# Kernel optimization log

Measured on AMD Instinct MI355X. Metric: run time of the kernel, lower is better.

## Reference

```python
import jax, jax.numpy as jnp
import numpy as np

B, A, DIN, HID, HEADS, NOUT, K = 256, 64, 64, 128, 4, 2, 7
N = B * A                      # 16384 nodes
C = HID                        # per-head dim == out_channels (module quirk)
SCALE = (HID // HEADS) ** -0.5 # 1/sqrt(32), as in the module


def _xavier(k, shape):
    fan_out, fan_in = shape
    lim = (6.0 / (fan_in + fan_out)) ** 0.5
    return jax.random.uniform(k, shape, jnp.float32, -lim, lim)


def setup_inputs() -> dict:
    key = jax.random.key(0)
    ks = jax.random.split(key, 24)
    x = jax.random.normal(ks[0], (N, DIN), jnp.float32)
    pos_b = jax.random.uniform(ks[1], (B, A, 2), jnp.float32) * 10.0  # [B,A,2]
    pos = pos_b.reshape(N, 2)

    # kNN graph per environment (replicates torch.cdist + topk smallest, drop self)
    d = jnp.linalg.norm(pos_b[:, :, None, :] - pos_b[:, None, :, :], axis=-1)  # [B,A,A]
    _, idx = jax.lax.top_k(-d, K + 1)
    nb = idx[..., 1:]                                   # [B,A,K] neighbor ids
    offs = (jnp.arange(B) * A)[:, None, None]
    src = jnp.broadcast_to(jnp.arange(A)[None, :, None], (B, A, K)) + offs
    dst = nb + offs
    loops = jnp.arange(N)
    edge_index = jnp.stack([
        jnp.concatenate([src.reshape(-1), loops]),
        jnp.concatenate([dst.reshape(-1), loops]),
    ]).astype(jnp.int32)                                # [2, E], E = B*A*K + N

    inp = {"x": x, "pos": pos, "edge_index": edge_index}
    inp["l0_Wq"] = _xavier(ks[2], (HEADS * C, 2))
    inp["l0_Wk"] = _xavier(ks[3], (HEADS * C, 2))
    inp["l0_Wv"] = _xavier(ks[4], (HEADS * C, DIN))
    inp["l0_Wo"] = _xavier(ks[5], (HID, HEADS * C))
    inp["l0_bo"] = jnp.zeros((HID,), jnp.float32)
    inp["l1_Wq"] = _xavier(ks[6], (HEADS * C, 2))
    inp["l1_Wk"] = _xavier(ks[7], (HEADS * C, 2))
    inp["l1_Wv"] = _xavier(ks[8], (HEADS * C, HID))
    inp["l1_Wo"] = _xavier(ks[9], (HID, HEADS * C))
    inp["l1_bo"] = jnp.zeros((HID,), jnp.float32)
    inp["W1"] = _xavier(ks[10], (256, HID))
    inp["b1"] = jnp.zeros((256,), jnp.float32)
    inp["W2"] = _xavier(ks[11], (256, 256))
    inp["b2"] = jnp.zeros((256,), jnp.float32)
    inp["W3"] = _xavier(ks[12], (NOUT, 256))
    inp["b3"] = jnp.zeros((NOUT,), jnp.float32)
    return inp


def _gat(x, pos, src, dst, Wq, Wk, Wv, Wo, bo):
    # positions -> Q/K, features -> V (position-aware attention)
    q = (pos @ Wq.T).reshape(N, HEADS, C)
    k = (pos @ Wk.T).reshape(N, HEADS, C)
    v = (x @ Wv.T).reshape(N, HEADS, C)
    # per-edge logits, segment softmax over incoming edges of dst
    alpha = jnp.einsum('ehc,ehc->eh', q[dst], k[src]) * SCALE        # [E,H]
    amax = jax.ops.segment_max(alpha, dst, num_segments=N)           # [N,H]
    ex = jnp.exp(alpha - amax[dst])
    a = ex / jax.ops.segment_sum(ex, dst, num_segments=N)[dst]
    msg = v[src] * a[..., None]                                      # [E,H,C]
    agg = jax.ops.segment_sum(msg, dst, num_segments=N)              # [N,H,C]
    return agg.reshape(N, HEADS * C) @ Wo.T + bo


def reference(x, pos, edge_index,
              l0_Wq, l0_Wk, l0_Wv, l0_Wo, l0_bo,
              l1_Wq, l1_Wk, l1_Wv, l1_Wo, l1_bo,
              W1, b1, W2, b2, W3, b3):
    src, dst = edge_index[0], edge_index[1]
    h = jnp.tanh(_gat(x, pos, src, dst, l0_Wq, l0_Wk, l0_Wv, l0_Wo, l0_bo))
    h = jnp.tanh(_gat(h, pos, src, dst, l1_Wq, l1_Wk, l1_Wv, l1_Wo, l1_bo))
    h = jax.nn.relu(h @ W1.T + b1)
    h = jax.nn.relu(h @ W2.T + b2)
    out = h @ W3.T + b3
    return out.reshape(B, A, NOUT)
```

## Files before the change

kernel.cpp:

```cpp
#include <hip/hip_runtime.h>
#include <hip/hip_bf16.h>
#include <cstddef>
#include <math.h>

#define N_NODES 16384
#define DIN 64
#define HID 128
#define SCALE_F 0.17677669529663687f

using bf16x8 = __attribute__((ext_vector_type(8))) short;
using f32x4  = __attribute__((ext_vector_type(4))) float;

__device__ __forceinline__ ushort f2b(float x) {
  __hip_bfloat16 h = __float2bfloat16(x);
  return *(ushort*)&h;
}
__device__ __forceinline__ float b2f(ushort u) {
  __hip_bfloat16 h = *(__hip_bfloat16*)&u;
  return __bfloat162float(h);
}
__device__ __forceinline__ void split1(float x, ushort& h, ushort& l) {
  h = f2b(x);
  l = f2b(x - b2f(h));
}
__device__ __forceinline__ void split3(float x, ushort& a, ushort& b, ushort& c) {
  a = f2b(x);
  float r1 = x - b2f(a);
  b = f2b(r1);
  c = f2b(r1 - b2f(b));
}

#define MFMA(d, A, B) d = __builtin_amdgcn_mfma_f32_16x16x32_bf16(A, B, d, 0, 0, 0)


__global__ __launch_bounds__(256) void prep_all_kernel(
    const float* __restrict__ Wq0, const float* __restrict__ Wk0,
    const float* __restrict__ Wq1, const float* __restrict__ Wk1,
    float* __restrict__ G,
    const float* __restrict__ Wv0, const float* __restrict__ Wo0,
    ushort* __restrict__ M0a, ushort* __restrict__ M0b, ushort* __restrict__ M0c,
    const float* __restrict__ Wv1, const float* __restrict__ Wo1,
    ushort* __restrict__ M1a, ushort* __restrict__ M1b, ushort* __restrict__ M1c,
    const float* __restrict__ W1, ushort* __restrict__ W1hi, ushort* __restrict__ W1lo,
    const float* __restrict__ W2, ushort* __restrict__ W2hi, ushort* __restrict__ W2lo,
    unsigned long long* __restrict__ out64)
{
  int blk = blockIdx.x, t = threadIdx.x;
  if (blk == 0) {
    if (t >= 32) return;
    int l = t >> 4, h = (t >> 2) & 3, a = (t >> 1) & 1, b = t & 1;
    const float* Wq = l ? Wq1 : Wq0;
    const float* Wk = l ? Wk1 : Wk0;
    float acc = 0.f;
    for (int c = 0; c < 128; c++)
      acc += Wq[(h * 128 + c) * 2 + a] * Wk[(h * 128 + c) * 2 + b];
    G[t] = acc;
  } else if (blk < 385) {
    int D, idx;
    const float *Wv, *Wo;
    ushort *Ma, *Mb, *Mc;
    if (blk < 129) { D = DIN; idx = (blk - 1) * 256 + t; Wv = Wv0; Wo = Wo0; Ma = M0a; Mb = M0b; Mc = M0c; }
    else           { D = HID; idx = (blk - 129) * 256 + t; Wv = Wv1; Wo = Wo1; Ma = M1a; Mb = M1b; Mc = M1c; }
    int K4 = 4 * D;
    int o = idx / K4, hd = idx - o * K4;
    int h = hd / D, d = hd - h * D;
    const float* wv = Wv + (size_t)(h * 128) * D + d;
    const float* wo = Wo + (size_t)o * 512 + h * 128;
    float acc = 0.f;
    for (int c = 0; c < 128; c++)
      acc += wv[(size_t)c * D] * wo[c];
    split3(acc, Ma[idx], Mb[idx], Mc[idx]);
  } else if (blk < 769) {
    int i = (blk - 385) * 256 + t;
    if (i < 256 * 128) split1(W1[i], W1hi[i], W1lo[i]);
    int j = i - 256 * 128;
    if (j >= 0 && j < 256 * 256) split1(W2[j], W2hi[j], W2lo[j]);
  } else {
    int i = (blk - 769) * 256 + t;
    if (i < N_NODES) out64[i] = 0ull;
  }
}


#define SFB_OFF 8192
#define SFC_OFF 16384
#define PXS_OFF 24576
#define PYS_OFF 24704
#define SMASK_OFF 24832
#define AFRAG_OFF 25088
#define PH_OFF 57856
#define LDS_USHORTS 74752

template <int KD>
__device__ __forceinline__ void gat_layer(
    int wave, int lane, int lm, int lq,
    const ushort* sFa, const ushort* sFb, const ushort* sFc,
    ushort* aA,
    const float* pxs, const float* pys,
    const unsigned long long* smask,
    const float* __restrict__ G,
    const ushort* __restrict__ Ma, const ushort* __restrict__ Mb,
    const ushort* __restrict__ Mc,
    f32x4 hacc[4])
{
  {
    int wm = wave & 3;
    int h = wave >> 2;
    float pdxm = pxs[wm * 16 + lm];
    float pdym = pys[wm * 16 + lm];
    unsigned long long mm = smask[wm * 16 + lm];
    unsigned mb0 = (unsigned)((mm >> (8 * lq)) & 0xFF);
    unsigned mb1 = (unsigned)((mm >> (32 + 8 * lq)) & 0xFF);
    float g0 = G[h * 4], g1 = G[h * 4 + 1], g2 = G[h * 4 + 2], g3 = G[h * 4 + 3];
    float a0 = (g0 * pdxm + g2 * pdym) * SCALE_F;
    float a1 = (g1 * pdxm + g3 * pdym) * SCALE_F;
    float sshift = a0 * pdxm + a1 * pdym;
    float e[16];
    float sum = 0.f;
#pragma unroll
    for (int j = 0; j < 8; j++) {
      e[j]     = ((mb0 >> j) & 1) ? __expf(a0 * pxs[8 * lq + j] + a1 * pys[8 * lq + j] - sshift) : 0.f;
      e[8 + j] = ((mb1 >> j) & 1) ? __expf(a0 * pxs[32 + 8 * lq + j] + a1 * pys[32 + 8 * lq + j] - sshift) : 0.f;
      sum += e[j] + e[8 + j];
    }
    sum += __shfl_xor(sum, 16);
    sum += __shfl_xor(sum, 32);
    float inv = 1.f / sum;
    bf16x8 Aa0, Aa1, Ab0, Ab1;
#pragma unroll
    for (int j = 0; j < 8; j++) {
      ushort ua, ub;
      split1(e[j] * inv, ua, ub);     Aa0[j] = (short)ua; Ab0[j] = (short)ub;
      split1(e[8 + j] * inv, ua, ub); Aa1[j] = (short)ua; Ab1[j] = (short)ub;
    }
    int sbase = wave * 2048 + lane * 8;
    *(bf16x8*)&aA[sbase]        = Aa0;
    *(bf16x8*)&aA[sbase + 512]  = Aa1;
    *(bf16x8*)&aA[sbase + 1024] = Ab0;
    *(bf16x8*)&aA[sbase + 1536] = Ab1;
  }
  __syncthreads();

  const int K4 = 4 * KD;
  const int o = 16 * (wave & 7) + lm;
  const int hb = wave >> 3;
#pragma unroll
  for (int i = 0; i < 4; i++) hacc[i] = (f32x4){0.f, 0.f, 0.f, 0.f};

#pragma unroll 1
  for (int hi = 0; hi < 2; hi++) {
    int h = 2 * hb + hi;
    f32x4 y[4];
#pragma unroll
    for (int i = 0; i < 4; i++) y[i] = (f32x4){0.f, 0.f, 0.f, 0.f};
#pragma unroll 1
    for (int kf = 0; kf < KD / 32; kf++) {
      size_t boff = (size_t)o * K4 + h * KD + kf * 32 + lq * 8;
      bf16x8 ma = *(const bf16x8*)&Ma[boff];
      bf16x8 mb = *(const bf16x8*)&Mb[boff];
      bf16x8 mc = *(const bf16x8*)&Mc[boff];
      int ko = kf * 32 + lq * 8;
      int sw = lm << 3;
#pragma unroll
      for (int mp = 0; mp < 2; mp++) {
        int f0 = (mp * 32 + lm) * 128 + (ko ^ sw);
        int f1 = f0 + 16 * 128;
        bf16x8 fa0 = *(const bf16x8*)&sFa[f0], fa1 = *(const bf16x8*)&sFa[f1];
        bf16x8 fb0 = *(const bf16x8*)&sFb[f0], fb1 = *(const bf16x8*)&sFb[f1];
        bf16x8 fc0 = *(const bf16x8*)&sFc[f0], fc1 = *(const bf16x8*)&sFc[f1];
        f32x4 y0 = y[mp * 2], y1 = y[mp * 2 + 1];
        MFMA(y0, fa0, ma); MFMA(y1, fa1, ma);
        MFMA(y0, fa0, mb); MFMA(y1, fa1, mb);
        MFMA(y0, fb0, ma); MFMA(y1, fb1, ma);
        MFMA(y0, fa0, mc); MFMA(y1, fa1, mc);
        MFMA(y0, fc0, ma); MFMA(y1, fc1, ma);
        MFMA(y0, fb0, mb); MFMA(y1, fb1, mb);
        y[mp * 2] = y0; y[mp * 2 + 1] = y1;
      }
    }
    bf16x8 Ya[2], Yb[2];
#pragma unroll
    for (int kb = 0; kb < 2; kb++) {
#pragma unroll
      for (int j = 0; j < 8; j++) {
        int sl = ((2 * lq + (j >> 2)) & 3) * 16 + lm;
        float v0 = __shfl(y[2 * kb][j & 3], sl);
        float v1 = __shfl(y[2 * kb + 1][j & 3], sl);
        float v = (lq & 2) ? v1 : v0;
        ushort ua, ub;
        split1(v, ua, ub);
        Ya[kb][j] = (short)ua; Yb[kb][j] = (short)ub;
      }
    }
#pragma unroll
    for (int mtd = 0; mtd < 4; mtd++) {
      int abase = (h * 4 + mtd) * 2048 + lane * 8;
      bf16x8 Aa0 = *(const bf16x8*)&aA[abase];
      bf16x8 Aa1 = *(const bf16x8*)&aA[abase + 512];
      bf16x8 Ab0 = *(const bf16x8*)&aA[abase + 1024];
      bf16x8 Ab1 = *(const bf16x8*)&aA[abase + 1536];
      MFMA(hacc[mtd], Aa0, Ya[0]);
      MFMA(hacc[mtd], Aa0, Yb[0]);
      MFMA(hacc[mtd], Ab0, Ya[0]);
      MFMA(hacc[mtd], Ab0, Yb[0]);
      MFMA(hacc[mtd], Aa1, Ya[1]);
      MFMA(hacc[mtd], Aa1, Yb[1]);
      MFMA(hacc[mtd], Ab1, Ya[1]);
      MFMA(hacc[mtd], Ab1, Yb[1]);
    }
  }
}

__global__ __attribute__((amdgpu_flat_work_group_size(1024, 1024), amdgpu_waves_per_eu(4)))
void fused_gat_kernel(
    const float* __restrict__ x, const float* __restrict__ pos,
    const int* __restrict__ srcp, const int* __restrict__ dstp,
    const float* __restrict__ G,
    const ushort* __restrict__ M0a, const ushort* __restrict__ M0b, const ushort* __restrict__ M0c,
    const ushort* __restrict__ M1a, const ushort* __restrict__ M1b, const ushort* __restrict__ M1c,
    const float* __restrict__ bo0, const float* __restrict__ bo1,
    const ushort* __restrict__ W1hi, const ushort* __restrict__ W1lo, const float* __restrict__ b1,
    const ushort* __restrict__ W2hi, const ushort* __restrict__ W2lo, const float* __restrict__ b2,
    const float* __restrict__ W3, const float* __restrict__ b3,
    float* __restrict__ outp)
{
  __shared__ __align__(16) ushort uBig[LDS_USHORTS];
  ushort* sFa = uBig;
  ushort* sFb = uBig + SFB_OFF;
  ushort* sFc = uBig + SFC_OFF;
  float* pxs = (float*)(uBig + PXS_OFF);
  float* pys = (float*)(uBig + PYS_OFF);
  unsigned long long* smask = (unsigned long long*)(uBig + SMASK_OFF);
  ushort* aA = uBig + AFRAG_OFF;
  ushort* pA = uBig + AFRAG_OFF;
  ushort* pB = uBig + AFRAG_OFF + 16384;
  float* pH = (float*)(uBig + PH_OFF);

  int b = blockIdx.x, t = threadIdx.x;
  int wave = t >> 6, lane = t & 63, lm = lane & 15, lq = lane >> 4;

  if (t < 64) {
    pxs[t] = pos[(b * 64 + t) * 2];
    pys[t] = pos[(b * 64 + t) * 2 + 1];
    smask[t] = 1ull << t;
  }
  {
    const float4* gx = (const float4*)(x + (size_t)b * 64 * DIN);
    float4 v = gx[t];
    int r = t >> 4, c = (t & 15) * 4;
    int cs = c ^ ((r & 15) << 3);
    ushort4 ua, ub, uc;
    split3(v.x, ua.x, ub.x, uc.x); split3(v.y, ua.y, ub.y, uc.y);
    split3(v.z, ua.z, ub.z, uc.z); split3(v.w, ua.w, ub.w, uc.w);
    *(ushort4*)&sFa[r * 128 + cs] = ua;
    *(ushort4*)&sFb[r * 128 + cs] = ub;
    *(ushort4*)&sFc[r * 128 + cs] = uc;
  }
  __syncthreads();
  if (t < 448) {
    int s = srcp[b * 448 + t];
    int d = dstp[b * 448 + t];
    atomicOr(&smask[d & 63], 1ull << (s & 63));
  }
  __syncthreads();

  f32x4 hacc[4];
  gat_layer<DIN>(wave, lane, lm, lq, sFa, sFb, sFc, aA, pxs, pys, smask,
                 G, M0a, M0b, M0c, hacc);
  int o = 16 * (wave & 7) + lm;
  if (wave >= 8) {
#pragma unroll
    for (int mtd = 0; mtd < 4; mtd++)
#pragma unroll
      for (int r = 0; r < 4; r++)
        pH[(mtd * 16 + lq * 4 + r) * 132 + o] = hacc[mtd][r];
  }
  __syncthreads();
  if (wave < 8) {
    float bv = bo0[o];
#pragma unroll
    for (int mtd = 0; mtd < 4; mtd++)
#pragma unroll
      for (int r = 0; r < 4; r++) {
        int dst = mtd * 16 + lq * 4 + r;
        float v = tanhf(hacc[mtd][r] + pH[dst * 132 + o] + bv);
        ushort ua, ub, uc;
        split3(v, ua, ub, uc);
        int cs = o ^ ((dst & 15) << 3);
        sFa[dst * 128 + cs] = ua;
        sFb[dst * 128 + cs] = ub;
        sFc[dst * 128 + cs] = uc;
      }
  }
  __syncthreads();
  gat_layer<HID>(wave, lane, lm, lq, sFa, sFb, sFc, aA, pxs, pys, smask,
                 G + 16, M1a, M1b, M1c, hacc);
  if (wave >= 8) {
#pragma unroll
    for (int mtd = 0; mtd < 4; mtd++)
#pragma unroll
      for (int r = 0; r < 4; r++)
        pH[(mtd * 16 + lq * 4 + r) * 132 + o] = hacc[mtd][r];
  }
  __syncthreads();
  if (wave < 8) {
    float bv = bo1[o];
#pragma unroll
    for (int mtd = 0; mtd < 4; mtd++)
#pragma unroll
      for (int r = 0; r < 4; r++) {
        int dst = mtd * 16 + lq * 4 + r;
        float v = tanhf(hacc[mtd][r] + pH[dst * 132 + o] + bv);
        ushort hh, ll;
        split1(v, hh, ll);
        int cs = o ^ ((dst & 15) << 3);
        sFa[dst * 128 + cs] = hh;
        sFb[dst * 128 + cs] = ll;
      }
  }
  __syncthreads();
  f32x4 y1[4];
#pragma unroll
  for (int mtd = 0; mtd < 4; mtd++) y1[mtd] = (f32x4){0.f, 0.f, 0.f, 0.f};
#pragma unroll 1
  for (int kf = 0; kf < 4; kf++) {
    int ko = kf * 32 + lq * 8;
    int col = 16 * wave + lm;
    bf16x8 bh = *(const bf16x8*)&W1hi[(size_t)col * 128 + ko];
    bf16x8 bl = *(const bf16x8*)&W1lo[(size_t)col * 128 + ko];
#pragma unroll
    for (int mtd = 0; mtd < 4; mtd++) {
      int row = mtd * 16 + lm;
      int cs = ko ^ (lm << 3);
      bf16x8 ah = *(const bf16x8*)&sFa[row * 128 + cs];
      bf16x8 al = *(const bf16x8*)&sFb[row * 128 + cs];
      MFMA(y1[mtd], ah, bh);
      MFMA(y1[mtd], ah, bl);
      MFMA(y1[mtd], al, bh);
    }
  }
  {
    int col = 16 * wave + lm;
    float bv = b1[col];
#pragma unroll
    for (int mtd = 0; mtd < 4; mtd++)
#pragma unroll
      for (int r = 0; r < 4; r++) {
        int row = mtd * 16 + lq * 4 + r;
        float v = fmaxf(y1[mtd][r] + bv, 0.f);
        ushort hh, ll;
        split1(v, hh, ll);
        int cc = col ^ ((row & 15) << 3);
        pA[row * 256 + cc] = hh;
        pB[row * 256 + cc] = ll;
      }
  }
  __syncthreads();
  f32x4 y2[4];
#pragma unroll
  for (int mtd = 0; mtd < 4; mtd++) y2[mtd] = (f32x4){0.f, 0.f, 0.f, 0.f};
#pragma unroll 1
  for (int kf = 0; kf < 8; kf++) {
    int ko = kf * 32 + lq * 8;
    bf16x8 bh = *(const bf16x8*)&W2hi[(size_t)(16 * wave + lm) * 256 + ko];
    bf16x8 bl = *(const bf16x8*)&W2lo[(size_t)(16 * wave + lm) * 256 + ko];
#pragma unroll
    for (int mtd = 0; mtd < 4; mtd++) {
      int row = mtd * 16 + lm;
      int cc = ko ^ (lm << 3);
      bf16x8 ah = *(const bf16x8*)&pA[row * 256 + cc];
      bf16x8 al = *(const bf16x8*)&pB[row * 256 + cc];
      MFMA(y2[mtd], ah, bh);
      MFMA(y2[mtd], ah, bl);
      MFMA(y2[mtd], al, bh);
    }
  }
  {
    int c0 = 16 * wave + lm;
    float w30 = W3[c0], w31 = W3[256 + c0];
    float b20 = b2[c0];
    float bb0 = (wave == 0) ? b3[0] : 0.f;
    float bb1 = (wave == 0) ? b3[1] : 0.f;
#pragma unroll
    for (int mtd = 0; mtd < 4; mtd++)
#pragma unroll
      for (int r = 0; r < 4; r++) {
        float va = fmaxf(y2[mtd][r] + b20, 0.f);
        float s0 = va * w30;
        float s1 = va * w31;
        s0 += __shfl_xor(s0, 1); s0 += __shfl_xor(s0, 2);
        s0 += __shfl_xor(s0, 4); s0 += __shfl_xor(s0, 8);
        s1 += __shfl_xor(s1, 1); s1 += __shfl_xor(s1, 2);
        s1 += __shfl_xor(s1, 4); s1 += __shfl_xor(s1, 8);
        if (lm == 0) {
          int row = b * 64 + mtd * 16 + lq * 4 + r;
          atomicAdd(&outp[row * 2 + 0], s0 + bb0);
          atomicAdd(&outp[row * 2 + 1], s1 + bb1);
        }
      }
  }
}


extern "C" void kernel_launch(void* const* d_in, const int* in_sizes, int n_in,
                              void* d_out, int out_size, void* d_ws, size_t ws_size,
                              hipStream_t stream) {
  const float* x     = (const float*)d_in[0];
  const float* pos   = (const float*)d_in[1];
  const int*   ei    = (const int*)d_in[2];
  const float* l0_Wq = (const float*)d_in[3];
  const float* l0_Wk = (const float*)d_in[4];
  const float* l0_Wv = (const float*)d_in[5];
  const float* l0_Wo = (const float*)d_in[6];
  const float* l0_bo = (const float*)d_in[7];
  const float* l1_Wq = (const float*)d_in[8];
  const float* l1_Wk = (const float*)d_in[9];
  const float* l1_Wv = (const float*)d_in[10];
  const float* l1_Wo = (const float*)d_in[11];
  const float* l1_bo = (const float*)d_in[12];
  const float* W1    = (const float*)d_in[13];
  const float* b1    = (const float*)d_in[14];
  const float* W2    = (const float*)d_in[15];
  const float* b2    = (const float*)d_in[16];
  const float* W3    = (const float*)d_in[17];
  const float* b3    = (const float*)d_in[18];
  float* outp = (float*)d_out;

  int E = in_sizes[2] / 2;
  const int* srcp = ei;
  const int* dstp = ei + E;

  char* base = (char*)d_ws;
  size_t off = 0;
  auto alloc = [&](size_t bytes) -> void* {
    void* p = base + off;
    off = (off + bytes + 255) & ~(size_t)255;
    return p;
  };
  float*  G   = (float*)alloc(32 * sizeof(float));
  ushort* M0a = (ushort*)alloc((size_t)128 * 256 * 2);
  ushort* M0b = (ushort*)alloc((size_t)128 * 256 * 2);
  ushort* M0c = (ushort*)alloc((size_t)128 * 256 * 2);
  ushort* M1a = (ushort*)alloc((size_t)128 * 512 * 2);
  ushort* M1b = (ushort*)alloc((size_t)128 * 512 * 2);
  ushort* M1c = (ushort*)alloc((size_t)128 * 512 * 2);
  ushort* W1hi = (ushort*)alloc((size_t)256 * 128 * 2);
  ushort* W1lo = (ushort*)alloc((size_t)256 * 128 * 2);
  ushort* W2hi = (ushort*)alloc((size_t)256 * 256 * 2);
  ushort* W2lo = (ushort*)alloc((size_t)256 * 256 * 2);

  prep_all_kernel<<<833, 256, 0, stream>>>(
      l0_Wq, l0_Wk, l1_Wq, l1_Wk, G,
      l0_Wv, l0_Wo, M0a, M0b, M0c,
      l1_Wv, l1_Wo, M1a, M1b, M1c,
      W1, W1hi, W1lo, W2, W2hi, W2lo,
      (unsigned long long*)outp);

  fused_gat_kernel<<<N_NODES / 64, 1024, 0, stream>>>(
      x, pos, srcp, dstp, G, M0a, M0b, M0c, M1a, M1b, M1c, l0_bo, l1_bo,
      W1hi, W1lo, b1, W2hi, W2lo, b2, W3, b3, outp);

  (void)n_in; (void)out_size; (void)ws_size;
}
```

Baseline: 151.7 us.

## Prefetch weight fragments into registers ahead of barriers and MFMA loops

Global loads of the per-layer attention weight fragments, MLP weights, biases, edge lists, positions and input features are moved earlier. They are issued before barriers or softmax work and held in registers, and the K loops are fully unrolled. The head-1 weights of each GAT layer are prefetched right after the head-0 MFMAs finish. The aim is to hide global-memory latency behind compute and barriers, at the cost of much higher VGPR pressure that may cut occupancy or cause spills.

```diff
diff --git a/kernel.cpp b/kernel.cpp
--- a/kernel.cpp
+++ b/kernel.cpp
@@ -103,6 +103,20 @@
     const ushort* __restrict__ Mc,
     f32x4 hacc[4])
 {
+  constexpr int NKF = KD / 32;
+  const int K4 = 4 * KD;
+  const int o = 16 * (wave & 7) + lm;
+  const int hb = wave >> 3;
+
+  bf16x8 pmA[NKF], pmB[NKF], pmC[NKF];
+#pragma unroll
+  for (int kf = 0; kf < NKF; kf++) {
+    size_t boff = (size_t)o * K4 + (2 * hb) * KD + kf * 32 + lq * 8;
+    pmA[kf] = *(const bf16x8*)&Ma[boff];
+    pmB[kf] = *(const bf16x8*)&Mb[boff];
+    pmC[kf] = *(const bf16x8*)&Mc[boff];
+  }
+
   {
     int wm = wave & 3;
     int h = wave >> 2;
@@ -141,9 +155,6 @@
   }
   __syncthreads();
 
-  const int K4 = 4 * KD;
-  const int o = 16 * (wave & 7) + lm;
-  const int hb = wave >> 3;
 #pragma unroll
   for (int i = 0; i < 4; i++) hacc[i] = (f32x4){0.f, 0.f, 0.f, 0.f};
 
@@ -153,12 +164,11 @@
     f32x4 y[4];
 #pragma unroll
     for (int i = 0; i < 4; i++) y[i] = (f32x4){0.f, 0.f, 0.f, 0.f};
-#pragma unroll 1
-    for (int kf = 0; kf < KD / 32; kf++) {
-      size_t boff = (size_t)o * K4 + h * KD + kf * 32 + lq * 8;
-      bf16x8 ma = *(const bf16x8*)&Ma[boff];
-      bf16x8 mb = *(const bf16x8*)&Mb[boff];
-      bf16x8 mc = *(const bf16x8*)&Mc[boff];
+#pragma unroll
+    for (int kf = 0; kf < NKF; kf++) {
+      bf16x8 ma = pmA[kf];
+      bf16x8 mb = pmB[kf];
+      bf16x8 mc = pmC[kf];
       int ko = kf * 32 + lq * 8;
       int sw = lm << 3;
 #pragma unroll
@@ -176,6 +186,15 @@
         MFMA(y0, fc0, ma); MFMA(y1, fc1, ma);
         MFMA(y0, fb0, mb); MFMA(y1, fb1, mb);
         y[mp * 2] = y0; y[mp * 2 + 1] = y1;
+      }
+    }
+    if (hi == 0) {
+#pragma unroll
+      for (int kf = 0; kf < NKF; kf++) {
+        size_t boff = (size_t)o * K4 + (2 * hb + 1) * KD + kf * 32 + lq * 8;
+        pmA[kf] = *(const bf16x8*)&Ma[boff];
+        pmB[kf] = *(const bf16x8*)&Mb[boff];
+        pmC[kf] = *(const bf16x8*)&Mc[boff];
       }
     }
     bf16x8 Ya[2], Yb[2];
@@ -238,36 +257,47 @@
 
   int b = blockIdx.x, t = threadIdx.x;
   int wave = t >> 6, lane = t & 63, lm = lane & 15, lq = lane >> 4;
-
+  int o = 16 * (wave & 7) + lm;
+
+  int e_s = 0, e_d = 0;
+  if (t < 448) {
+    e_s = srcp[b * 448 + t];
+    e_d = dstp[b * 448 + t];
+  }
+  float posx = 0.f, posy = 0.f;
   if (t < 64) {
-    pxs[t] = pos[(b * 64 + t) * 2];
-    pys[t] = pos[(b * 64 + t) * 2 + 1];
+    posx = pos[(b * 64 + t) * 2];
+    posy = pos[(b * 64 + t) * 2 + 1];
+  }
+  const float4* gx = (const float4*)(x + (size_t)b * 64 * DIN);
+  float4 xv = gx[t];
+  float bv0 = bo0[o];
+  float bv1 = bo1[o];
+
+  if (t < 64) {
+    pxs[t] = posx;
+    pys[t] = posy;
     smask[t] = 1ull << t;
   }
   {
-    const float4* gx = (const float4*)(x + (size_t)b * 64 * DIN);
-    float4 v = gx[t];
     int r = t >> 4, c = (t & 15) * 4;
     int cs = c ^ ((r & 15) << 3);
     ushort4 ua, ub, uc;
-    split3(v.x, ua.x, ub.x, uc.x); split3(v.y, ua.y, ub.y, uc.y);
-    split3(v.z, ua.z, ub.z, uc.z); split3(v.w, ua.w, ub.w, uc.w);
+    split3(xv.x, ua.x, ub.x, uc.x); split3(xv.y, ua.y, ub.y, uc.y);
+    split3(xv.z, ua.z, ub.z, uc.z); split3(xv.w, ua.w, ub.w, uc.w);
     *(ushort4*)&sFa[r * 128 + cs] = ua;
     *(ushort4*)&sFb[r * 128 + cs] = ub;
     *(ushort4*)&sFc[r * 128 + cs] = uc;
   }
   __syncthreads();
   if (t < 448) {
-    int s = srcp[b * 448 + t];
-    int d = dstp[b * 448 + t];
-    atomicOr(&smask[d & 63], 1ull << (s & 63));
+    atomicOr(&smask[e_d & 63], 1ull << (e_s & 63));
   }
   __syncthreads();
 
   f32x4 hacc[4];
   gat_layer<DIN>(wave, lane, lm, lq, sFa, sFb, sFc, aA, pxs, pys, smask,
                  G, M0a, M0b, M0c, hacc);
-  int o = 16 * (wave & 7) + lm;
   if (wave >= 8) {
 #pragma unroll
     for (int mtd = 0; mtd < 4; mtd++)
@@ -277,13 +307,12 @@
   }
   __syncthreads();
   if (wave < 8) {
-    float bv = bo0[o];
 #pragma unroll
     for (int mtd = 0; mtd < 4; mtd++)
 #pragma unroll
       for (int r = 0; r < 4; r++) {
         int dst = mtd * 16 + lq * 4 + r;
-        float v = tanhf(hacc[mtd][r] + pH[dst * 132 + o] + bv);
+        float v = tanhf(hacc[mtd][r] + pH[dst * 132 + o] + bv0);
         ushort ua, ub, uc;
         split3(v, ua, ub, uc);
         int cs = o ^ ((dst & 15) << 3);
@@ -295,6 +324,17 @@
   __syncthreads();
   gat_layer<HID>(wave, lane, lm, lq, sFa, sFb, sFc, aA, pxs, pys, smask,
                  G + 16, M1a, M1b, M1c, hacc);
+
+  int col = 16 * wave + lm;
+  bf16x8 pw1h[4], pw1l[4];
+#pragma unroll
+  for (int kf = 0; kf < 4; kf++) {
+    int ko = kf * 32 + lq * 8;
+    pw1h[kf] = *(const bf16x8*)&W1hi[(size_t)col * 128 + ko];
+    pw1l[kf] = *(const bf16x8*)&W1lo[(size_t)col * 128 + ko];
+  }
+  float b1v = b1[col];
+
   if (wave >= 8) {
 #pragma unroll
     for (int mtd = 0; mtd < 4; mtd++)
@@ -304,13 +344,12 @@
   }
   __syncthreads();
   if (wave < 8) {
-    float bv = bo1[o];
 #pragma unroll
     for (int mtd = 0; mtd < 4; mtd++)
 #pragma unroll
       for (int r = 0; r < 4; r++) {
         int dst = mtd * 16 + lq * 4 + r;
-        float v = tanhf(hacc[mtd][r] + pH[dst * 132 + o] + bv);
+        float v = tanhf(hacc[mtd][r] + pH[dst * 132 + o] + bv1);
         ushort hh, ll;
         split1(v, hh, ll);
         int cs = o ^ ((dst & 15) << 3);
@@ -322,12 +361,11 @@
   f32x4 y1[4];
 #pragma unroll
   for (int mtd = 0; mtd < 4; mtd++) y1[mtd] = (f32x4){0.f, 0.f, 0.f, 0.f};
-#pragma unroll 1
+#pragma unroll
   for (int kf = 0; kf < 4; kf++) {
     int ko = kf * 32 + lq * 8;
-    int col = 16 * wave + lm;
-    bf16x8 bh = *(const bf16x8*)&W1hi[(size_t)col * 128 + ko];
-    bf16x8 bl = *(const bf16x8*)&W1lo[(size_t)col * 128 + ko];
+    bf16x8 bh = pw1h[kf];
+    bf16x8 bl = pw1l[kf];
 #pragma unroll
     for (int mtd = 0; mtd < 4; mtd++) {
       int row = mtd * 16 + lm;
@@ -340,14 +378,12 @@
     }
   }
   {
-    int col = 16 * wave + lm;
-    float bv = b1[col];
 #pragma unroll
     for (int mtd = 0; mtd < 4; mtd++)
 #pragma unroll
       for (int r = 0; r < 4; r++) {
         int row = mtd * 16 + lq * 4 + r;
-        float v = fmaxf(y1[mtd][r] + bv, 0.f);
+        float v = fmaxf(y1[mtd][r] + b1v, 0.f);
         ushort hh, ll;
         split1(v, hh, ll);
         int cc = col ^ ((row & 15) << 3);
@@ -355,15 +391,26 @@
         pB[row * 256 + cc] = ll;
       }
   }
-  __syncthreads();
-  f32x4 y2[4];
-#pragma unroll
-  for (int mtd = 0; mtd < 4; mtd++) y2[mtd] = (f32x4){0.f, 0.f, 0.f, 0.f};
-#pragma unroll 1
+  bf16x8 pw2h[8], pw2l[8];
+#pragma unroll
   for (int kf = 0; kf < 8; kf++) {
     int ko = kf * 32 + lq * 8;
-    bf16x8 bh = *(const bf16x8*)&W2hi[(size_t)(16 * wave + lm) * 256 + ko];
-    bf16x8 bl = *(const bf16x8*)&W2lo[(size_t)(16 * wave + lm) * 256 + ko];
+    pw2h[kf] = *(const bf16x8*)&W2hi[(size_t)col * 256 + ko];
+    pw2l[kf] = *(const bf16x8*)&W2lo[(size_t)col * 256 + ko];
+  }
+  float w30 = W3[col], w31 = W3[256 + col];
+  float b20 = b2[col];
+  float bb0 = (wave == 0) ? b3[0] : 0.f;
+  float bb1 = (wave == 0) ? b3[1] : 0.f;
+  __syncthreads();
+  f32x4 y2[4];
+#pragma unroll
+  for (int mtd = 0; mtd < 4; mtd++) y2[mtd] = (f32x4){0.f, 0.f, 0.f, 0.f};
+#pragma unroll
+  for (int kf = 0; kf < 8; kf++) {
+    int ko = kf * 32 + lq * 8;
+    bf16x8 bh = pw2h[kf];
+    bf16x8 bl = pw2l[kf];
 #pragma unroll
     for (int mtd = 0; mtd < 4; mtd++) {
       int row = mtd * 16 + lm;
@@ -376,11 +423,6 @@
     }
   }
   {
-    int c0 = 16 * wave + lm;
-    float w30 = W3[c0], w31 = W3[256 + c0];
-    float b20 = b2[c0];
-    float bb0 = (wave == 0) ? b3[0] : 0.f;
-    float bb1 = (wave == 0) ? b3[1] : 0.f;
 #pragma unroll
     for (int mtd = 0; mtd < 4; mtd++)
 #pragma unroll
```

Result: slower. 265.6 us (+75.1%).
